# Optimization experiments

Measured on AMD Instinct MI355X. Metric: run time of the kernel, lower is better.

## Reference

```python
import jax, jax.numpy as jnp
import numpy as np

# --- NAVAR dims (from init_kwargs) ---
ND, NS, NV, HID = 2, 4, 12, 16      # n_datasets, n_samples, n_variables, hidden_dim
GROUPS = ND * NS * NV               # 96 independent grouped-conv streams
K = 4                               # kernel_size
NBLOCKS = 3                         # dilated blocks, dilations 1,2,4
B, T = 8, 2048                      # batch, sequence length


def causal_conv(x, w, b, dilation, groups):
    """Grouped causal dilated 1D conv. x:(B,C,T), w:(O, C//groups, K), b:(O,)."""
    pad = (w.shape[-1] - 1) * dilation
    y = jax.lax.conv_general_dilated(
        x, w, window_strides=(1,), padding=[(pad, 0)],
        rhs_dilation=(dilation,),
        dimension_numbers=("NCH", "OIH", "NCH"),
        feature_group_count=groups,
    )
    return y + b[None, :, None]


def setup_inputs() -> dict:
    key = jax.random.key(0)
    ks = jax.random.split(key, 5)
    s = lambda fan_in: np.float32(1.0 / np.sqrt(fan_in))
    x = jax.random.normal(ks[0], (B, ND, NS, NV, T), dtype=jnp.float32)
    # grouped input conv: 1 -> HID channels per group
    w_in = jax.random.normal(ks[1], (GROUPS * HID, 1, K), dtype=jnp.float32) * s(K)
    b_in = jnp.zeros((GROUPS * HID,), jnp.float32)
    # dilated hidden blocks: HID -> HID per group
    w_h = jax.random.normal(ks[2], (NBLOCKS, GROUPS * HID, HID, K), dtype=jnp.float32) * s(HID * K)
    b_h = jnp.zeros((NBLOCKS, GROUPS * HID), jnp.float32)
    # grouped 1x1 output conv: HID -> NV contributions per group
    w_out = jax.random.normal(ks[3], (GROUPS * NV, HID, 1), dtype=jnp.float32) * s(HID)
    b_out = jnp.zeros((GROUPS * NV,), jnp.float32)
    # NAVAR additive biases (init 0.01 as in torch code)
    biases = jnp.full((1, ND, NS, NV, 1), 0.01, jnp.float32)
    return dict(x=x, w_in=w_in, b_in=b_in, w_h=w_h, b_h=b_h,
                w_out=w_out, b_out=b_out, biases=biases)


def reference(x, w_in, b_in, w_h, b_h, w_out, b_out, biases):
    batch = x.shape[0]
    h = x.reshape(batch, GROUPS, T)                       # (B, groups, T)
    h = jax.nn.relu(causal_conv(h, w_in, b_in, 1, GROUPS))
    for i in range(NBLOCKS):                              # fixed small loop over layers
        h = jax.nn.relu(causal_conv(h, w_h[i], b_h[i], 2 ** i, GROUPS))
    c = causal_conv(h, w_out, b_out, 1, GROUPS)           # (B, groups*NV, T)
    c = c.reshape(batch, ND, NS, NV, NV, T)               # (B, nd, ns, src, dst, T)
    prediction = c.sum(axis=-3) + biases                  # sum over source variables
    contributions = jnp.swapaxes(c, -2, -3)               # (B, nd, ns, dst, src, T)
    return prediction, contributions
```

## Files before the change

kernel.cpp:

```cpp
#include <hip/hip_runtime.h>

#define T_LEN   2048
#define BATCH   8
#define HIDDEN  16
#define KSZ     4
#define NVAR    12
#define NGROUPS 96
#define TILE_OUT 232
#define BUF     256
#define HALO    24
#define NTILES  9
#define PAD     16
#define NROWS   (BUF + PAD)
#define ROWCH   24

#define NWH  (3 * NGROUPS * HIDDEN * HIDDEN * KSZ)
#define NWO  (NGROUPS * HIDDEN * 32)

typedef __attribute__((ext_vector_type(8))) short bf16x8;
typedef __attribute__((ext_vector_type(4))) float f32x4;

__device__ __forceinline__ unsigned short f2bf(float x) {
    union { float f; unsigned u; } v; v.f = x;
    unsigned r = v.u + 0x7FFFu + ((v.u >> 16) & 1u);
    return (unsigned short)(r >> 16);
}

__global__ __launch_bounds__(256) void navar_pack(
        const float* __restrict__ w_h, const float* __restrict__ w_out,
        unsigned short* __restrict__ wp, unsigned short* __restrict__ wpo) {
    const int e = blockIdx.x * 256 + threadIdx.x;
    if (e < NWH) {
        const int k  = e & 63, row = e >> 6;
        const int kk = k >> 4, i = k & 15;
        wp[e] = f2bf(w_h[(row << 6) + i * 4 + kk]);
    } else {
        const int e2 = e - NWH;
        const int k = e2 & 31, m = (e2 >> 5) & 15, g = e2 >> 9;
        wpo[e2] = (k < 16 && m < 12) ? f2bf(w_out[(g * NVAR + m) * HIDDEN + k])
                                     : (unsigned short)0;
    }
}

template<int D>
__device__ __forceinline__ void mfma_layer(
        const unsigned short (*__restrict__ src)[ROWCH],
        unsigned short (*__restrict__ dst)[ROWCH],
        const bf16x8 a0, const bf16x8 a1, const f32x4 bias,
        int tile, int wv, int q, int c) {
    const int ch = (q & 1) * 8;
    const int d0 = (3 - (q >> 1)) * D;
    const int d1 = (1 - (q >> 1)) * D;

    #pragma unroll
    for (int tt = 0; tt < 4; ++tt) {
        const int pos = (wv * 4 + tt) * 16 + c;
        const bf16x8 b0 = *(const bf16x8*)&src[PAD + pos - d0][ch];
        const bf16x8 b1 = *(const bf16x8*)&src[PAD + pos - d1][ch];
        f32x4 acc = bias;
        acc = __builtin_amdgcn_mfma_f32_16x16x32_bf16(a0, b0, acc, 0, 0, 0);
        acc = __builtin_amdgcn_mfma_f32_16x16x32_bf16(a1, b1, acc, 0, 0, 0);
        const int tgp = tile * TILE_OUT + pos - HALO;
        union { unsigned short s[4]; uint2 u; } pk;
        #pragma unroll
        for (int r = 0; r < 4; ++r)
            pk.s[r] = (tgp >= 0) ? f2bf(fmaxf(acc[r], 0.f)) : (unsigned short)0;
        *(uint2*)&dst[PAD + pos][q * 4] = pk.u;
    }
}

__global__ __launch_bounds__(256, 6) void navar_main(
        const float* __restrict__ x,
        const float* __restrict__ w_in,  const float* __restrict__ b_in,
        const unsigned short* __restrict__ wp, const float* __restrict__ b_h,
        const unsigned short* __restrict__ wpo, const float* __restrict__ b_out,
        float* __restrict__ contrib) {
    __shared__ unsigned short hb[2][NROWS][ROWCH];
    float* xs = (float*)&hb[1][0][0];

    const int p    = threadIdx.x;
    const int tile = blockIdx.x % NTILES;
    const int sg   = blockIdx.x / NTILES;
    const int b    = sg / NGROUPS;
    const int g    = sg % NGROUPS;
    const int tg   = tile * TILE_OUT + p - HALO;

    const int wv = p >> 6, q = (p >> 4) & 3, c = p & 15;

    const size_t wstep = (size_t)NGROUPS * HIDDEN * (HIDDEN * KSZ);
    const unsigned short* wr0 =
        wp + (size_t)(g * HIDDEN + c) * (HIDDEN * KSZ);
    bf16x8 A0[3], A1[3]; f32x4 BH[3];
    #pragma unroll
    for (int l = 0; l < 3; ++l) {
        A0[l] = *(const bf16x8*)(wr0 + l * wstep + q * 8);
        A1[l] = *(const bf16x8*)(wr0 + l * wstep + 32 + q * 8);
        BH[l] = *(const f32x4*)(b_h + (l * NGROUPS + g) * HIDDEN + q * 4);
    }
    const unsigned short* wrowo = wpo + (size_t)(g * HIDDEN + c) * 32;
    const bf16x8 AO = *(const bf16x8*)(wrowo + q * 8);
    f32x4 BO = {0.f, 0.f, 0.f, 0.f};
    if (q < 3) BO = *(const f32x4*)(b_out + g * NVAR + q * 4);

    float xv = 0.f;
    if (tg >= 0 && tg < T_LEN) xv = x[(size_t)(b * NGROUPS + g) * T_LEN + tg];
    xs[p] = xv;
    __syncthreads();

    if (p >= 3) {
        const float t0 = xs[p-3], t1 = xs[p-2], t2 = xs[p-1], t3 = xs[p];
        const float* w  = w_in + g * HIDDEN * KSZ;
        const float* bb = b_in + g * HIDDEN;
        unsigned pk[8];
        #pragma unroll
        for (int o = 0; o < HIDDEN; ++o) {
            float acc = fmaf(w[o*4+0], t0, bb[o]);
            acc = fmaf(w[o*4+1], t1, acc);
            acc = fmaf(w[o*4+2], t2, acc);
            acc = fmaf(w[o*4+3], t3, acc);
            const unsigned short h =
                (tg >= 0) ? f2bf(fmaxf(acc, 0.f)) : (unsigned short)0;
            if (o & 1) pk[o >> 1] |= ((unsigned)h) << 16;
            else       pk[o >> 1] = h;
        }
        uint4* row = (uint4*)&hb[0][PAD + p][0];
        row[0] = make_uint4(pk[0], pk[1], pk[2], pk[3]);
        row[1] = make_uint4(pk[4], pk[5], pk[6], pk[7]);
    }
    __syncthreads();

    mfma_layer<1>(hb[0], hb[1], A0[0], A1[0], BH[0], tile, wv, q, c);
    __syncthreads();
    mfma_layer<2>(hb[1], hb[0], A0[1], A1[1], BH[1], tile, wv, q, c);
    __syncthreads();
    mfma_layer<4>(hb[0], hb[1], A0[2], A1[2], BH[2], tile, wv, q, c);
    __syncthreads();

    {
        const int gds = g / NVAR, srcv = g % NVAR;
        #pragma unroll
        for (int tt = 0; tt < 4; ++tt) {
            const int pos = (wv * 4 + tt) * 16 + c;
            const bf16x8 b0 = *(const bf16x8*)&hb[1][PAD + pos][(q & 1) * 8];
            f32x4 acc = BO;
            acc = __builtin_amdgcn_mfma_f32_16x16x32_bf16(AO, b0, acc, 0, 0, 0);
            const int tgp = tile * TILE_OUT + pos - HALO;
            if (q < 3 && pos >= HALO && tgp < T_LEN) {
                const size_t base =
                    (((size_t)b * NGROUPS + gds * NVAR) * NVAR + srcv) * T_LEN + tgp;
                #pragma unroll
                for (int r = 0; r < 4; ++r)
                    contrib[base + (size_t)(q * 4 + r) * NVAR * T_LEN] = acc[r];
            }
        }
    }
}

__global__ __launch_bounds__(256) void navar_pred(
        const float* __restrict__ contrib, const float* __restrict__ biases,
        float* __restrict__ pred) {
    const int e = (blockIdx.x * 256 + threadIdx.x) * 4;
    const int t = e % T_LEN;
    const int G = e / T_LEN;
    const float4* c = (const float4*)(contrib + (size_t)G * NVAR * T_LEN + t);
    const float bias = biases[G % NGROUPS];
    float4 acc = make_float4(bias, bias, bias, bias);
    #pragma unroll
    for (int s = 0; s < NVAR; ++s) {
        float4 v = c[(size_t)s * (T_LEN / 4)];
        acc.x += v.x; acc.y += v.y; acc.z += v.z; acc.w += v.w;
    }
    *(float4*)(pred + e) = acc;
}

extern "C" void kernel_launch(void* const* d_in, const int* in_sizes, int n_in,
                              void* d_out, int out_size, void* d_ws, size_t ws_size,
                              hipStream_t stream) {
    const float* x      = (const float*)d_in[0];
    const float* w_in   = (const float*)d_in[1];
    const float* b_in   = (const float*)d_in[2];
    const float* w_h    = (const float*)d_in[3];
    const float* b_h    = (const float*)d_in[4];
    const float* w_out  = (const float*)d_in[5];
    const float* b_out  = (const float*)d_in[6];
    const float* biases = (const float*)d_in[7];

    float* pred    = (float*)d_out;
    float* contrib = pred + (size_t)BATCH * NGROUPS * T_LEN;
    unsigned short* wp  = (unsigned short*)d_ws;
    unsigned short* wpo = wp + NWH;

    navar_pack<<<(NWH + NWO) / 256, 256, 0, stream>>>(w_h, w_out, wp, wpo);
    navar_main<<<BATCH * NGROUPS * NTILES, 256, 0, stream>>>(
        x, w_in, b_in, wp, b_h, wpo, b_out, contrib);
    navar_pred<<<(BATCH * NGROUPS * T_LEN) / (256 * 4), 256, 0, stream>>>(
        contrib, biases, pred);
}
```

Baseline: 146.5 us.

## Fuse weight packing into main kernel and use hardware bf16 pack conversion

Removes the separate weight-packing kernel launch. Each block now reads the fp32 hidden and output weights directly and converts them to bf16 MFMA operands in registers using v_cvt_pk_bf16_f32. The software rounding helper is replaced with the same hardware packed conversion, and the input-conv staging through shared memory plus its barrier is replaced by wavefront shuffles, with the first three lanes of each wave reloading their halo values from global memory. This trades one launch and a global round trip for redundant fp32 weight loads and conversions in every block.

New measurement: 198.1 us. +35.2%, slower.

```diff
diff --git a/kernel.cpp b/kernel.cpp
--- a/kernel.cpp
+++ b/kernel.cpp
@@ -14,32 +14,13 @@
 #define NROWS   (BUF + PAD)
 #define ROWCH   24
 
-#define NWH  (3 * NGROUPS * HIDDEN * HIDDEN * KSZ)
-#define NWO  (NGROUPS * HIDDEN * 32)
-
 typedef __attribute__((ext_vector_type(8))) short bf16x8;
 typedef __attribute__((ext_vector_type(4))) float f32x4;
 
-__device__ __forceinline__ unsigned short f2bf(float x) {
-    union { float f; unsigned u; } v; v.f = x;
-    unsigned r = v.u + 0x7FFFu + ((v.u >> 16) & 1u);
-    return (unsigned short)(r >> 16);
-}
-
-__global__ __launch_bounds__(256) void navar_pack(
-        const float* __restrict__ w_h, const float* __restrict__ w_out,
-        unsigned short* __restrict__ wp, unsigned short* __restrict__ wpo) {
-    const int e = blockIdx.x * 256 + threadIdx.x;
-    if (e < NWH) {
-        const int k  = e & 63, row = e >> 6;
-        const int kk = k >> 4, i = k & 15;
-        wp[e] = f2bf(w_h[(row << 6) + i * 4 + kk]);
-    } else {
-        const int e2 = e - NWH;
-        const int k = e2 & 31, m = (e2 >> 5) & 15, g = e2 >> 9;
-        wpo[e2] = (k < 16 && m < 12) ? f2bf(w_out[(g * NVAR + m) * HIDDEN + k])
-                                     : (unsigned short)0;
-    }
+__device__ __forceinline__ unsigned cvtpk(float lo, float hi) {
+    unsigned r;
+    asm("v_cvt_pk_bf16_f32 %0, %1, %2" : "=v"(r) : "v"(lo), "v"(hi));
+    return r;
 }
 
 template<int D>
@@ -61,22 +42,21 @@
         acc = __builtin_amdgcn_mfma_f32_16x16x32_bf16(a0, b0, acc, 0, 0, 0);
         acc = __builtin_amdgcn_mfma_f32_16x16x32_bf16(a1, b1, acc, 0, 0, 0);
         const int tgp = tile * TILE_OUT + pos - HALO;
-        union { unsigned short s[4]; uint2 u; } pk;
-        #pragma unroll
-        for (int r = 0; r < 4; ++r)
-            pk.s[r] = (tgp >= 0) ? f2bf(fmaxf(acc[r], 0.f)) : (unsigned short)0;
-        *(uint2*)&dst[PAD + pos][q * 4] = pk.u;
+        uint2 pku;
+        pku.x = cvtpk(fmaxf(acc[0], 0.f), fmaxf(acc[1], 0.f));
+        pku.y = cvtpk(fmaxf(acc[2], 0.f), fmaxf(acc[3], 0.f));
+        if (tgp < 0) { pku.x = 0u; pku.y = 0u; }
+        *(uint2*)&dst[PAD + pos][q * 4] = pku;
     }
 }
 
 __global__ __launch_bounds__(256, 6) void navar_main(
         const float* __restrict__ x,
         const float* __restrict__ w_in,  const float* __restrict__ b_in,
-        const unsigned short* __restrict__ wp, const float* __restrict__ b_h,
-        const unsigned short* __restrict__ wpo, const float* __restrict__ b_out,
+        const float* __restrict__ w_h,   const float* __restrict__ b_h,
+        const float* __restrict__ w_out, const float* __restrict__ b_out,
         float* __restrict__ contrib) {
     __shared__ unsigned short hb[2][NROWS][ROWCH];
-    float* xs = (float*)&hb[1][0][0];
 
     const int p    = threadIdx.x;
     const int tile = blockIdx.x % NTILES;
@@ -86,42 +66,68 @@
     const int tg   = tile * TILE_OUT + p - HALO;
 
     const int wv = p >> 6, q = (p >> 4) & 3, c = p & 15;
-
-    const size_t wstep = (size_t)NGROUPS * HIDDEN * (HIDDEN * KSZ);
-    const unsigned short* wr0 =
-        wp + (size_t)(g * HIDDEN + c) * (HIDDEN * KSZ);
+    const int kk = q >> 1;
+
     bf16x8 A0[3], A1[3]; f32x4 BH[3];
     #pragma unroll
     for (int l = 0; l < 3; ++l) {
-        A0[l] = *(const bf16x8*)(wr0 + l * wstep + q * 8);
-        A1[l] = *(const bf16x8*)(wr0 + l * wstep + 32 + q * 8);
+        const float* wrow = w_h
+            + ((size_t)((l * NGROUPS + g) * HIDDEN + c) << 6) + (q & 1) * 32;
+        float a0f[8], a1f[8];
+        #pragma unroll
+        for (int j = 0; j < 8; ++j) {
+            const float4 v4 = *(const float4*)(wrow + 4 * j);
+            a0f[j] = kk ? v4.y : v4.x;
+            a1f[j] = kk ? v4.w : v4.z;
+        }
+        union { uint4 u; bf16x8 h; } r0, r1;
+        r0.u = make_uint4(cvtpk(a0f[0], a0f[1]), cvtpk(a0f[2], a0f[3]),
+                          cvtpk(a0f[4], a0f[5]), cvtpk(a0f[6], a0f[7]));
+        r1.u = make_uint4(cvtpk(a1f[0], a1f[1]), cvtpk(a1f[2], a1f[3]),
+                          cvtpk(a1f[4], a1f[5]), cvtpk(a1f[6], a1f[7]));
+        A0[l] = r0.h; A1[l] = r1.h;
         BH[l] = *(const f32x4*)(b_h + (l * NGROUPS + g) * HIDDEN + q * 4);
     }
-    const unsigned short* wrowo = wpo + (size_t)(g * HIDDEN + c) * 32;
-    const bf16x8 AO = *(const bf16x8*)(wrowo + q * 8);
+    union { uint4 u; bf16x8 h; } ro;
+    ro.u = make_uint4(0u, 0u, 0u, 0u);
+    if (q < 2 && c < NVAR) {
+        const float* wo = w_out + (size_t)(g * NVAR + c) * HIDDEN + q * 8;
+        const float4 v0 = *(const float4*)(wo);
+        const float4 v1 = *(const float4*)(wo + 4);
+        ro.u = make_uint4(cvtpk(v0.x, v0.y), cvtpk(v0.z, v0.w),
+                          cvtpk(v1.x, v1.y), cvtpk(v1.z, v1.w));
+    }
+    const bf16x8 AO = ro.h;
     f32x4 BO = {0.f, 0.f, 0.f, 0.f};
     if (q < 3) BO = *(const f32x4*)(b_out + g * NVAR + q * 4);
 
-    float xv = 0.f;
-    if (tg >= 0 && tg < T_LEN) xv = x[(size_t)(b * NGROUPS + g) * T_LEN + tg];
-    xs[p] = xv;
-    __syncthreads();
-
+    const size_t xrow = (size_t)(b * NGROUPS + g) * T_LEN;
+    const float xv = (tg >= 0 && tg < T_LEN) ? x[xrow + tg] : 0.f;
+    float t2 = __shfl_up(xv, 1);
+    float t1 = __shfl_up(xv, 2);
+    float t0 = __shfl_up(xv, 3);
     if (p >= 3) {
-        const float t0 = xs[p-3], t1 = xs[p-2], t2 = xs[p-1], t3 = xs[p];
+        if ((p & 63) < 3) {
+            t0 = (tg >= 3 && tg - 3 < T_LEN) ? x[xrow + tg - 3] : 0.f;
+            t1 = (tg >= 2 && tg - 2 < T_LEN) ? x[xrow + tg - 2] : 0.f;
+            t2 = (tg >= 1 && tg - 1 < T_LEN) ? x[xrow + tg - 1] : 0.f;
+        }
+        const float t3 = xv;
         const float* w  = w_in + g * HIDDEN * KSZ;
         const float* bb = b_in + g * HIDDEN;
         unsigned pk[8];
         #pragma unroll
-        for (int o = 0; o < HIDDEN; ++o) {
-            float acc = fmaf(w[o*4+0], t0, bb[o]);
-            acc = fmaf(w[o*4+1], t1, acc);
-            acc = fmaf(w[o*4+2], t2, acc);
-            acc = fmaf(w[o*4+3], t3, acc);
-            const unsigned short h =
-                (tg >= 0) ? f2bf(fmaxf(acc, 0.f)) : (unsigned short)0;
-            if (o & 1) pk[o >> 1] |= ((unsigned)h) << 16;
-            else       pk[o >> 1] = h;
+        for (int o = 0; o < HIDDEN; o += 2) {
+            float e0 = fmaf(w[o*4+0], t0, bb[o]);
+            e0 = fmaf(w[o*4+1], t1, e0);
+            e0 = fmaf(w[o*4+2], t2, e0);
+            e0 = fmaf(w[o*4+3], t3, e0);
+            float e1 = fmaf(w[o*4+4], t0, bb[o+1]);
+            e1 = fmaf(w[o*4+5], t1, e1);
+            e1 = fmaf(w[o*4+6], t2, e1);
+            e1 = fmaf(w[o*4+7], t3, e1);
+            const unsigned u = cvtpk(fmaxf(e0, 0.f), fmaxf(e1, 0.f));
+            pk[o >> 1] = (tg >= 0) ? u : 0u;
         }
         uint4* row = (uint4*)&hb[0][PAD + p][0];
         row[0] = make_uint4(pk[0], pk[1], pk[2], pk[3]);
@@ -187,12 +193,10 @@
 
     float* pred    = (float*)d_out;
     float* contrib = pred + (size_t)BATCH * NGROUPS * T_LEN;
-    unsigned short* wp  = (unsigned short*)d_ws;
-    unsigned short* wpo = wp + NWH;
-
-    navar_pack<<<(NWH + NWO) / 256, 256, 0, stream>>>(w_h, w_out, wp, wpo);
+    (void)d_ws; (void)ws_size;
+
     navar_main<<<BATCH * NGROUPS * NTILES, 256, 0, stream>>>(
-        x, w_in, b_in, wp, b_h, wpo, b_out, contrib);
+        x, w_in, b_in, w_h, b_h, w_out, b_out, contrib);
     navar_pred<<<(BATCH * NGROUPS * T_LEN) / (256 * 4), 256, 0, stream>>>(
         contrib, biases, pred);
 }
```
